# Performance work log

Measured on AMD Instinct MI355X. Metric: run time of the kernel, lower is better.

## Reference

```python
import jax, jax.numpy as jnp
import numpy as np

N = 100000      # nodes
E = 1000000     # edges
H_DIM = 124     # node embedding dim
CLS_DIM = 4     # node class-logit dim (H_DIM + CLS_DIM = in_features = 128)
POLAR_DIM = 2   # edge_pred_features
HIDDEN = 256
OUT = 2
LN_EPS = 1e-5


def setup_inputs() -> dict:
    key = jax.random.key(0)
    ks = jax.random.split(key, 10)
    in_dim = 2 * (H_DIM + CLS_DIM) + POLAR_DIM  # 258
    return {
        "h": jax.random.normal(ks[0], (N, H_DIM), dtype=jnp.float32),
        "cls": jax.random.normal(ks[1], (N, CLS_DIM), dtype=jnp.float32),
        "polar": jax.random.normal(ks[2], (E, POLAR_DIM), dtype=jnp.float32),
        "src": jax.random.randint(ks[3], (E,), 0, N, dtype=jnp.int64),
        "dst": jax.random.randint(ks[4], (E,), 0, N, dtype=jnp.int64),
        # parameters (PyTorch Linear default-ish init scale)
        "W1": jax.random.normal(ks[5], (in_dim, HIDDEN), dtype=jnp.float32) * (1.0 / np.sqrt(in_dim)),
        "b1": jnp.zeros((HIDDEN,), dtype=jnp.float32),
        "gamma": jnp.ones((HIDDEN,), dtype=jnp.float32),
        "beta": jnp.zeros((HIDDEN,), dtype=jnp.float32),
        "W2": jax.random.normal(ks[6], (HIDDEN, OUT), dtype=jnp.float32) * (1.0 / np.sqrt(HIDDEN)),
        "b2": jnp.zeros((OUT,), dtype=jnp.float32),
    }


def reference(h, cls, polar, src, dst, W1, b1, gamma, beta, W2, b2):
    # softmax over class logits per node (same math as softmax on gathered
    # edge copies, but computed once per node)
    cls_sm = jax.nn.softmax(cls, axis=1)                  # [N, CLS_DIM]
    # gather src/dst node features along edges
    x = jnp.concatenate(
        [h[src], cls_sm[src], polar, h[dst], cls_sm[dst]], axis=1
    )                                                     # [E, 258]
    z = x @ W1 + b1                                        # [E, HIDDEN]
    # LayerNorm
    mu = jnp.mean(z, axis=-1, keepdims=True)
    var = jnp.mean(jnp.square(z - mu), axis=-1, keepdims=True)
    z = (z - mu) * jax.lax.rsqrt(var + LN_EPS) * gamma + beta
    z = jax.nn.relu(z)
    # dropout is identity in eval mode
    score = z @ W2 + b2                                    # [E, OUT]
    return score
```

## Files before the change

kernel.cpp:

```cpp
#include <hip/hip_runtime.h>
#include <hip/hip_bf16.h>

#define NN 100000
#define EE 1000000
#define H_DIM 124
#define PCOLS 512
#define LDK 136
#define CW 132

typedef float f32x4 __attribute__((ext_vector_type(4)));
typedef short bf16x8 __attribute__((ext_vector_type(8)));
typedef _Float16 h2 __attribute__((ext_vector_type(2)));

__device__ __forceinline__ unsigned short f2bf(float f) {
    unsigned int x = __float_as_uint(f);
    unsigned int r = (x + 0x7FFFu + ((x >> 16) & 1u)) >> 16;
    return (unsigned short)r;
}
__device__ __forceinline__ unsigned int pk2bf(float a, float b) {
    return (unsigned int)f2bf(a) | ((unsigned int)f2bf(b) << 16);
}
__device__ __forceinline__ unsigned int pk2h(float a, float b) {
    h2 v = (h2){(_Float16)a, (_Float16)b};
    return __builtin_bit_cast(unsigned int, v);
}

__device__ __forceinline__ float fdot2(h2 a, h2 b, float c) {
#if __has_builtin(__builtin_amdgcn_fdot2)
    return __builtin_amdgcn_fdot2(a, b, c, false);
#else
    return c + (float)a[0] * (float)b[0] + (float)a[1] * (float)b[1];
#endif
}

#if __has_builtin(__builtin_amdgcn_update_dpp)
template <int CTRL>
__device__ __forceinline__ float dpp_add(float x) {
    int xi = __builtin_bit_cast(int, x);
    int t = __builtin_amdgcn_update_dpp(xi, xi, CTRL, 0xF, 0xF, false);
    return x + __builtin_bit_cast(float, t);
}
__device__ __forceinline__ float reduce16(float x) {
    x = dpp_add<0x128>(x);
    x = dpp_add<0x124>(x);
    x = dpp_add<0x122>(x);
    x = dpp_add<0x121>(x);
    return x;
}
#else
__device__ __forceinline__ float reduce16(float x) {
    x += __shfl_xor(x, 8); x += __shfl_xor(x, 4);
    x += __shfl_xor(x, 2); x += __shfl_xor(x, 1);
    return x;
}
#endif

struct alignas(16) H8 { h2 p[4]; };

__global__ __launch_bounds__(256) void build_w1t(const float* __restrict__ W1,
                                                 unsigned short* __restrict__ W1T) {
    int t2 = blockIdx.x * 256 + threadIdx.x;
    int j = t2 >> 7, k = t2 & 127;
    int row = (j < 256) ? k : (130 + k);
    int col = (j < 256) ? j : (j - 256);
    W1T[t2] = f2bf(W1[row * 256 + col]);
}

__global__ __launch_bounds__(256) void p_gemm(const float* __restrict__ h,
                                              const float* __restrict__ cls,
                                              const unsigned short* __restrict__ W1T,
                                              const float* __restrict__ b1,
                                              _Float16* __restrict__ P) {
    __shared__ alignas(16) unsigned short As[64 * LDK];
    __shared__ alignas(16) unsigned short Bs[128 * LDK];
    float* Cs = (float*)&Bs[0];
    const int m0 = blockIdx.x * 64;
    const int t = threadIdx.x;

    #pragma unroll
    for (int it = 0; it < 4; ++it) {
        int chunk = t + it * 256;
        int r = chunk >> 4, c8 = chunk & 15;
        int row = m0 + r;
        unsigned int w0 = 0, w1 = 0, w2 = 0, w3 = 0;
        if (row < NN) {
            if (c8 < 15) {
                const float* hp = h + (size_t)row * H_DIM + c8 * 8;
                float4 v0 = *(const float4*)(hp);
                float4 v1 = *(const float4*)(hp + 4);
                w0 = pk2bf(v0.x, v0.y); w1 = pk2bf(v0.z, v0.w);
                w2 = pk2bf(v1.x, v1.y); w3 = pk2bf(v1.z, v1.w);
            } else {
                float4 v0 = *(const float4*)(h + (size_t)row * H_DIM + 120);
                float4 c = *(const float4*)(cls + (size_t)row * 4);
                float m = fmaxf(fmaxf(c.x, c.y), fmaxf(c.z, c.w));
                float e0 = __expf(c.x - m), e1 = __expf(c.y - m);
                float e2 = __expf(c.z - m), e3 = __expf(c.w - m);
                float inv = 1.0f / (e0 + e1 + e2 + e3);
                w0 = pk2bf(v0.x, v0.y); w1 = pk2bf(v0.z, v0.w);
                w2 = pk2bf(e0 * inv, e1 * inv); w3 = pk2bf(e2 * inv, e3 * inv);
            }
        }
        *(uint4*)(&As[r * LDK + c8 * 8]) = make_uint4(w0, w1, w2, w3);
    }
    __syncthreads();

    const int wave = t >> 6, lane = t & 63;
    const int wm = wave & 1, wn = wave >> 1;
    const int lm = lane & 15, quad = lane >> 4;

    bf16x8 afrag[4][2];
    #pragma unroll
    for (int s = 0; s < 4; ++s) {
        int k0 = s * 32 + quad * 8;
        #pragma unroll
        for (int mt = 0; mt < 2; ++mt)
            afrag[s][mt] = *(const bf16x8*)(&As[(wm * 32 + mt * 16 + lm) * LDK + k0]);
    }

    for (int cchunk = 0; cchunk < 4; ++cchunk) {
        const int n0 = cchunk * 128;
        if (cchunk) __syncthreads();
        #pragma unroll
        for (int it = 0; it < 8; ++it) {
            int chunk = t + it * 256;
            int r = chunk >> 4, c = chunk & 15;
            float4 v = *(const float4*)(W1T + (n0 + r) * 128 + c * 8);
            *(float4*)(&Bs[r * LDK + c * 8]) = v;
        }
        __syncthreads();

        f32x4 acc[2][4];
        #pragma unroll
        for (int mt = 0; mt < 2; ++mt)
            #pragma unroll
            for (int nt = 0; nt < 4; ++nt)
                acc[mt][nt] = (f32x4){0.f, 0.f, 0.f, 0.f};

        #pragma unroll
        for (int s = 0; s < 4; ++s) {
            int k0 = s * 32 + quad * 8;
            bf16x8 b[4];
            #pragma unroll
            for (int nt = 0; nt < 4; ++nt)
                b[nt] = *(const bf16x8*)(&Bs[(wn * 64 + nt * 16 + lm) * LDK + k0]);
            #pragma unroll
            for (int mt = 0; mt < 2; ++mt)
                #pragma unroll
                for (int nt = 0; nt < 4; ++nt)
                    acc[mt][nt] = __builtin_amdgcn_mfma_f32_16x16x32_bf16(afrag[s][mt], b[nt], acc[mt][nt], 0, 0, 0);
        }
        __syncthreads();

        #pragma unroll
        for (int mt = 0; mt < 2; ++mt)
            #pragma unroll
            for (int nt = 0; nt < 4; ++nt) {
                int col = wn * 64 + nt * 16 + lm;
                int rb  = wm * 32 + mt * 16 + quad * 4;
                #pragma unroll
                for (int r = 0; r < 4; ++r)
                    Cs[(rb + r) * CW + col] = acc[mt][nt][r];
            }
        __syncthreads();

        #pragma unroll
        for (int it = 0; it < 4; ++it) {
            int chunk = t + it * 256;
            int r = chunk >> 4, c8 = chunk & 15;
            float4 a = *(const float4*)(Cs + r * CW + c8 * 8);
            float4 b = *(const float4*)(Cs + r * CW + c8 * 8 + 4);
            if (n0 >= 256) {
                int cb = n0 + c8 * 8 - 256;
                float4 ba = *(const float4*)(b1 + cb);
                float4 bb = *(const float4*)(b1 + cb + 4);
                a.x += ba.x; a.y += ba.y; a.z += ba.z; a.w += ba.w;
                b.x += bb.x; b.y += bb.y; b.z += bb.z; b.w += bb.w;
            }
            uint4 o = make_uint4(pk2h(a.x, a.y), pk2h(a.z, a.w),
                                 pk2h(b.x, b.y), pk2h(b.z, b.w));
            int row = m0 + r;
            if (row < NN)
                *(uint4*)(P + (size_t)row * PCOLS + n0 + c8 * 8) = o;
        }
    }
}

#define K3_BLOCKS 4096
#define K3_WAVES  (K3_BLOCKS * 4)
#define K3_STRIDE (K3_WAVES * 4)
#define K3_ROUNDS 16

struct EIdx { int s, d; float q0, q1; };

__device__ __forceinline__ EIdx load_idx(int eg, const int* __restrict__ src,
                                         const int* __restrict__ dst,
                                         const float* __restrict__ polar) {
    int ec = (eg < EE) ? eg : 0;
    EIdx r;
    r.s = src[ec]; r.d = dst[ec];
    float2 q = *(const float2*)(polar + 2 * ec);
    r.q0 = q.x; r.q1 = q.y;
    return r;
}

__device__ __forceinline__ void load_p(const _Float16* __restrict__ P, const EIdx& I,
                                       int il, H8* A) {
    const _Float16* ps = P + (size_t)I.s * PCOLS + il * 16;
    A[0] = *(const H8*)(ps);
    A[1] = *(const H8*)(ps + 8);
    const _Float16* pd = P + (size_t)I.d * PCOLS + 256 + il * 16;
    A[2] = *(const H8*)(pd);
    A[3] = *(const H8*)(pd + 8);
}

__global__ __launch_bounds__(256) void edge_kernel(const _Float16* __restrict__ P,
                                                   const int* __restrict__ src,
                                                   const int* __restrict__ dst,
                                                   const float* __restrict__ polar,
                                                   const float* __restrict__ W1,
                                                   const float* __restrict__ gamma,
                                                   const float* __restrict__ beta,
                                                   const float* __restrict__ W2,
                                                   const float* __restrict__ b2,
                                                   float* __restrict__ out) {
    const int lane = threadIdx.x & 63;
    const int il   = lane & 15;
    const int g    = lane >> 4;
    const int wid  = blockIdx.x * 4 + (threadIdx.x >> 6);
    const int jb   = il * 16;

    h2 w0c[8], w1c[8], gc[8], bc[8], w2ac[8], w2bc[8];
    #pragma unroll
    for (int p = 0; p < 8; ++p) {
        int j = jb + 2 * p;
        float2 a0 = *(const float2*)(W1 + 128 * 256 + j);
        float2 a1 = *(const float2*)(W1 + 129 * 256 + j);
        float2 ag = *(const float2*)(gamma + j);
        float2 ae = *(const float2*)(beta + j);
        float4 w2v = *(const float4*)(W2 + 2 * j);
        w0c[p]  = (h2){(_Float16)a0.x, (_Float16)a0.y};
        w1c[p]  = (h2){(_Float16)a1.x, (_Float16)a1.y};
        gc[p]   = (h2){(_Float16)ag.x, (_Float16)ag.y};
        bc[p]   = (h2){(_Float16)ae.x, (_Float16)ae.y};
        w2ac[p] = (h2){(_Float16)w2v.x, (_Float16)w2v.z};
        w2bc[p] = (h2){(_Float16)w2v.y, (_Float16)w2v.w};
    }
    const float b20 = b2[0], b21 = b2[1];
    const h2 onep  = (h2){(_Float16)1.0f, (_Float16)1.0f};
    const h2 zerop = (h2){(_Float16)0.0f, (_Float16)0.0f};

    const int e0 = wid * 4 + g;

    EIdx I0 = load_idx(e0, src, dst, polar);
    H8 A[4]; load_p(P, I0, il, A);
    EIdx I1 = load_idx(e0 + K3_STRIDE, src, dst, polar);
    H8 B[4]; load_p(P, I1, il, B);

    #define EDGE_COMPUTE(Abuf, Ix, eg)                                        \
    {                                                                          \
        h2 p0 = (h2){(_Float16)(Ix).q0, (_Float16)(Ix).q0};                    \
        h2 p1 = (h2){(_Float16)(Ix).q1, (_Float16)(Ix).q1};                    \
        h2 z[8];                                                               \
        float sum = 0.f, ss = 0.f;                                             \
        _Pragma("unroll")                                                      \
        for (int p = 0; p < 8; ++p) {                                          \
            h2 pv = ((p < 4) ? (Abuf)[0].p[p] : (Abuf)[1].p[p - 4])            \
                  + ((p < 4) ? (Abuf)[2].p[p] : (Abuf)[3].p[p - 4]);           \
            h2 c = w0c[p] * p0 + w1c[p] * p1;                                  \
            z[p] = pv + c;                                                     \
            sum = fdot2(z[p], onep, sum);                                      \
            ss  = fdot2(z[p], z[p], ss);                                       \
        }                                                                      \
        sum = reduce16(sum); ss = reduce16(ss);                                \
        float mu   = sum * (1.0f / 256.0f);                                    \
        float var  = ss * (1.0f / 256.0f) - mu * mu;                           \
        float rstd = rsqrtf(var + 1e-5f);                                      \
        h2 muh = (h2){(_Float16)mu, (_Float16)mu};                             \
        h2 rsh = (h2){(_Float16)rstd, (_Float16)rstd};                         \
        float o0 = 0.f, o1 = 0.f;                                              \
        _Pragma("unroll")                                                      \
        for (int p = 0; p < 8; ++p) {                                          \
            h2 tt = (z[p] - muh) * rsh;                                        \
            h2 u = tt * gc[p] + bc[p];                                         \
            u = __builtin_elementwise_max(u, zerop);                           \
            o0 = fdot2(u, w2ac[p], o0);                                        \
            o1 = fdot2(u, w2bc[p], o1);                                        \
        }                                                                      \
        o0 = reduce16(o0); o1 = reduce16(o1);                                  \
        if (il == 0 && (eg) < EE)                                              \
            *(float2*)(out + 2 * (eg)) = make_float2(o0 + b20, o1 + b21);      \
    }

    #pragma unroll
    for (int r = 0; r < K3_ROUNDS; r += 2) {
        EDGE_COMPUTE(A, I0, e0 + r * K3_STRIDE);
        if (r + 2 < K3_ROUNDS) {
            I0 = load_idx(e0 + (r + 2) * K3_STRIDE, src, dst, polar);
            load_p(P, I0, il, A);
        }
        EDGE_COMPUTE(B, I1, e0 + (r + 1) * K3_STRIDE);
        if (r + 3 < K3_ROUNDS) {
            I1 = load_idx(e0 + (r + 3) * K3_STRIDE, src, dst, polar);
            load_p(P, I1, il, B);
        }
    }
    #undef EDGE_COMPUTE
}

extern "C" void kernel_launch(void* const* d_in, const int* in_sizes, int n_in,
                              void* d_out, int out_size, void* d_ws, size_t ws_size,
                              hipStream_t stream) {
    const float* h     = (const float*)d_in[0];
    const float* cls   = (const float*)d_in[1];
    const float* polar = (const float*)d_in[2];
    const int*   src   = (const int*)d_in[3];
    const int*   dst   = (const int*)d_in[4];
    const float* W1    = (const float*)d_in[5];
    const float* b1    = (const float*)d_in[6];
    const float* gamma = (const float*)d_in[7];
    const float* beta  = (const float*)d_in[8];
    const float* W2    = (const float*)d_in[9];
    const float* b2    = (const float*)d_in[10];
    float* out = (float*)d_out;

    char* ws = (char*)d_ws;
    _Float16*       P   = (_Float16*)ws;
    unsigned short* W1T = (unsigned short*)(ws + 102400000);

    build_w1t<<<256, 256, 0, stream>>>(W1, W1T);
    p_gemm<<<1563, 256, 0, stream>>>(h, cls, W1T, b1, P);
    edge_kernel<<<K3_BLOCKS, 256, 0, stream>>>(P, src, dst, polar, W1, gamma, beta, W2, b2, out);
}
```

Measured before the change: 292.7 us.

## Triple-buffer edge gathers and precompute packed fp16 per-lane constants

The edge kernel moves from double-buffered to triple-buffered prefetch of gathered P rows and indices, keeping more gathers in flight per wave. Per-lane constants (the W1 polar rows, gamma, beta, W2) are pre-packed into fp16 by an extra block in the weight-prep kernel, so each edge-kernel thread loads 12 uint4 instead of doing strided fp32 loads and conversions. The LayerNorm normalization becomes a single FMA using a precomputed -mu*rstd. The third buffer adds register pressure, which could lower occupancy.

```diff
diff --git a/kernel.cpp b/kernel.cpp
--- a/kernel.cpp
+++ b/kernel.cpp
@@ -57,13 +57,39 @@
 
 struct alignas(16) H8 { h2 p[4]; };
 
-__global__ __launch_bounds__(256) void build_w1t(const float* __restrict__ W1,
-                                                 unsigned short* __restrict__ W1T) {
-    int t2 = blockIdx.x * 256 + threadIdx.x;
-    int j = t2 >> 7, k = t2 & 127;
-    int row = (j < 256) ? k : (130 + k);
-    int col = (j < 256) ? j : (j - 256);
-    W1T[t2] = f2bf(W1[row * 256 + col]);
+__global__ __launch_bounds__(256) void build_w1t_ct(const float* __restrict__ W1,
+                                                    const float* __restrict__ gamma,
+                                                    const float* __restrict__ beta,
+                                                    const float* __restrict__ W2,
+                                                    unsigned short* __restrict__ W1T,
+                                                    uint4* __restrict__ CT) {
+    if (blockIdx.x < 256) {
+        int t2 = blockIdx.x * 256 + threadIdx.x;
+        int j = t2 >> 7, k = t2 & 127;
+        int row = (j < 256) ? k : (130 + k);
+        int col = (j < 256) ? j : (j - 256);
+        W1T[t2] = f2bf(W1[row * 256 + col]);
+    } else {
+        int t = threadIdx.x;
+        if (t < 192) {
+            int slot = t % 12, il = t / 12;
+            int a = slot >> 1, k = slot & 1;
+            int j0 = il * 16 + k * 8;
+            float v[8];
+            #pragma unroll
+            for (int i = 0; i < 8; ++i) {
+                int j = j0 + i;
+                v[i] = (a == 0) ? W1[128 * 256 + j]
+                     : (a == 1) ? W1[129 * 256 + j]
+                     : (a == 2) ? gamma[j]
+                     : (a == 3) ? beta[j]
+                     : (a == 4) ? W2[2 * j]
+                     :            W2[2 * j + 1];
+            }
+            CT[t] = make_uint4(pk2h(v[0], v[1]), pk2h(v[2], v[3]),
+                               pk2h(v[4], v[5]), pk2h(v[6], v[7]));
+        }
+    }
 }
 
 __global__ __launch_bounds__(256) void p_gemm(const float* __restrict__ h,
@@ -218,33 +244,26 @@
                                                    const int* __restrict__ src,
                                                    const int* __restrict__ dst,
                                                    const float* __restrict__ polar,
-                                                   const float* __restrict__ W1,
-                                                   const float* __restrict__ gamma,
-                                                   const float* __restrict__ beta,
-                                                   const float* __restrict__ W2,
+                                                   const uint4* __restrict__ CT,
                                                    const float* __restrict__ b2,
                                                    float* __restrict__ out) {
     const int lane = threadIdx.x & 63;
     const int il   = lane & 15;
     const int g    = lane >> 4;
     const int wid  = blockIdx.x * 4 + (threadIdx.x >> 6);
-    const int jb   = il * 16;
-
+
+    uint4 cq[12];
+    #pragma unroll
+    for (int i = 0; i < 12; ++i) cq[i] = CT[il * 12 + i];
     h2 w0c[8], w1c[8], gc[8], bc[8], w2ac[8], w2bc[8];
-    #pragma unroll
-    for (int p = 0; p < 8; ++p) {
-        int j = jb + 2 * p;
-        float2 a0 = *(const float2*)(W1 + 128 * 256 + j);
-        float2 a1 = *(const float2*)(W1 + 129 * 256 + j);
-        float2 ag = *(const float2*)(gamma + j);
-        float2 ae = *(const float2*)(beta + j);
-        float4 w2v = *(const float4*)(W2 + 2 * j);
-        w0c[p]  = (h2){(_Float16)a0.x, (_Float16)a0.y};
-        w1c[p]  = (h2){(_Float16)a1.x, (_Float16)a1.y};
-        gc[p]   = (h2){(_Float16)ag.x, (_Float16)ag.y};
-        bc[p]   = (h2){(_Float16)ae.x, (_Float16)ae.y};
-        w2ac[p] = (h2){(_Float16)w2v.x, (_Float16)w2v.z};
-        w2bc[p] = (h2){(_Float16)w2v.y, (_Float16)w2v.w};
+    {
+        const h2* ch = (const h2*)cq;
+        #pragma unroll
+        for (int p = 0; p < 8; ++p) {
+            w0c[p]  = ch[p];      w1c[p]  = ch[8 + p];
+            gc[p]   = ch[16 + p]; bc[p]   = ch[24 + p];
+            w2ac[p] = ch[32 + p]; w2bc[p] = ch[40 + p];
+        }
     }
     const float b20 = b2[0], b21 = b2[1];
     const h2 onep  = (h2){(_Float16)1.0f, (_Float16)1.0f};
@@ -252,10 +271,13 @@
 
     const int e0 = wid * 4 + g;
 
-    EIdx I0 = load_idx(e0, src, dst, polar);
-    H8 A[4]; load_p(P, I0, il, A);
-    EIdx I1 = load_idx(e0 + K3_STRIDE, src, dst, polar);
-    H8 B[4]; load_p(P, I1, il, B);
+    EIdx I[3];
+    H8 buf[3][4];
+    #pragma unroll
+    for (int i = 0; i < 3; ++i) {
+        I[i] = load_idx(e0 + i * K3_STRIDE, src, dst, polar);
+        load_p(P, I[i], il, buf[i]);
+    }
 
     #define EDGE_COMPUTE(Abuf, Ix, eg)                                        \
     {                                                                          \
@@ -276,12 +298,13 @@
         float mu   = sum * (1.0f / 256.0f);                                    \
         float var  = ss * (1.0f / 256.0f) - mu * mu;                           \
         float rstd = rsqrtf(var + 1e-5f);                                      \
-        h2 muh = (h2){(_Float16)mu, (_Float16)mu};                             \
-        h2 rsh = (h2){(_Float16)rstd, (_Float16)rstd};                         \
+        float nmur = -mu * rstd;                                               \
+        h2 rsh  = (h2){(_Float16)rstd, (_Float16)rstd};                        \
+        h2 nmh  = (h2){(_Float16)nmur, (_Float16)nmur};                        \
         float o0 = 0.f, o1 = 0.f;                                              \
         _Pragma("unroll")                                                      \
         for (int p = 0; p < 8; ++p) {                                          \
-            h2 tt = (z[p] - muh) * rsh;                                        \
+            h2 tt = z[p] * rsh + nmh;                                          \
             h2 u = tt * gc[p] + bc[p];                                         \
             u = __builtin_elementwise_max(u, zerop);                           \
             o0 = fdot2(u, w2ac[p], o0);                                        \
@@ -293,16 +316,12 @@
     }
 
     #pragma unroll
-    for (int r = 0; r < K3_ROUNDS; r += 2) {
-        EDGE_COMPUTE(A, I0, e0 + r * K3_STRIDE);
-        if (r + 2 < K3_ROUNDS) {
-            I0 = load_idx(e0 + (r + 2) * K3_STRIDE, src, dst, polar);
-            load_p(P, I0, il, A);
-        }
-        EDGE_COMPUTE(B, I1, e0 + (r + 1) * K3_STRIDE);
+    for (int r = 0; r < K3_ROUNDS; ++r) {
+        const int br = r % 3;
+        EDGE_COMPUTE(buf[br], I[br], e0 + r * K3_STRIDE);
         if (r + 3 < K3_ROUNDS) {
-            I1 = load_idx(e0 + (r + 3) * K3_STRIDE, src, dst, polar);
-            load_p(P, I1, il, B);
+            I[br] = load_idx(e0 + (r + 3) * K3_STRIDE, src, dst, polar);
+            load_p(P, I[br], il, buf[br]);
         }
     }
     #undef EDGE_COMPUTE
@@ -327,8 +346,9 @@
     char* ws = (char*)d_ws;
     _Float16*       P   = (_Float16*)ws;
     unsigned short* W1T = (unsigned short*)(ws + 102400000);
-
-    build_w1t<<<256, 256, 0, stream>>>(W1, W1T);
+    uint4*          CT  = (uint4*)(ws + 102531072);
+
+    build_w1t_ct<<<257, 256, 0, stream>>>(W1, gamma, beta, W2, W1T, CT);
     p_gemm<<<1563, 256, 0, stream>>>(h, cls, W1T, b1, P);
-    edge_kernel<<<K3_BLOCKS, 256, 0, stream>>>(P, src, dst, polar, W1, gamma, beta, W2, b2, out);
-}
+    edge_kernel<<<K3_BLOCKS, 256, 0, stream>>>(P, src, dst, polar, CT, b2, out);
+}
```

Result: faster. 286.3 us (-2.2%).
